# Optimization experiments

Measured on AMD Instinct MI355X. Metric: run time of the kernel, lower is better.

The kernel has to match this reference:

```python
import jax, jax.numpy as jnp
import numpy as np

N_NETS = 76  # 29 h2o + 13 o3 + 9 co2 + 3 n2o + 9 ch4 + 13 u
N_CH = 29
N_KE = [29, 13, 9, 3, 9, 13]
# which composition column each of the 76 nets is scaled by
GAS_OF_NET = np.repeat(np.arange(6), N_KE)
# which output channel each of the 76 tau terms is added into (hardcoded table in subcall)
CHAN_OF_NET = np.concatenate([
    np.arange(29),                                            # h2o[i] -> channel i
    np.array([0, 1, 2, 17, 18, 19, 20, 21, 22, 25, 26, 27, 28]),  # o3
    np.array([0, 1, 2, 5, 6, 9, 10, 13, 14]),                 # co2
    np.array([0, 1, 2]),                                      # n2o
    np.array([0, 1, 2, 3, 4, 7, 8, 11, 12]),                  # ch4
    np.array([0, 1, 2, 15, 16, 17, 18, 19, 20, 21, 22, 27, 28]),  # u
])


def setup_inputs() -> dict:
    key = jax.random.key(0)
    ks = jax.random.split(key, 16)
    B, D_IN, H = 262144, 2, 4
    t_p = jax.random.normal(ks[0], (B, D_IN), dtype=jnp.float32)
    composition = jax.random.uniform(ks[1], (B, 8), dtype=jnp.float32)
    null_lw = jnp.zeros((B, 1), dtype=jnp.float32)
    null_iw = jnp.zeros((B, 1), dtype=jnp.float32)
    # stacked params of the 76 tiny DenseFFNs (hidden [4,4], elu; out 1, softplus)
    W1 = jax.random.normal(ks[2], (N_NETS, D_IN, H), dtype=jnp.float32) * 0.5
    b1 = jax.random.normal(ks[3], (N_NETS, H), dtype=jnp.float32) * 0.05
    W2 = jax.random.normal(ks[4], (N_NETS, H, H), dtype=jnp.float32) * 0.5
    b2 = jax.random.normal(ks[5], (N_NETS, H), dtype=jnp.float32) * 0.05
    W3 = jax.random.uniform(ks[6], (N_NETS, H, 1), minval=-1.0, maxval=1.0, dtype=jnp.float32)
    b3 = jnp.zeros((N_NETS, 1), dtype=jnp.float32)
    # per-channel lw / iw Dense(1) layers (input dim 1)
    W_lw = jax.random.normal(ks[7], (N_CH,), dtype=jnp.float32) * 0.5
    b_lw = jax.random.uniform(ks[8], (N_CH,), minval=0.0, maxval=1.0, dtype=jnp.float32)
    W_iw = jax.random.normal(ks[9], (N_CH,), dtype=jnp.float32) * 0.5
    b_iw = jax.random.uniform(ks[10], (N_CH,), minval=0.0, maxval=1.0, dtype=jnp.float32)
    return {"t_p": t_p, "composition": composition, "null_lw": null_lw, "null_iw": null_iw,
            "W1": W1, "b1": b1, "W2": W2, "b2": b2, "W3": W3, "b3": b3,
            "W_lw": W_lw, "b_lw": b_lw, "W_iw": W_iw, "b_iw": b_iw}


def reference(t_p, composition, null_lw, null_iw, W1, b1, W2, b2, W3, b3, W_lw, b_lw, W_iw, b_iw):
    # all 76 tiny MLPs batched as one einsum chain: [n_nets, B, h]
    h = jax.nn.elu(jnp.einsum('bi,nio->nbo', t_p, W1) + b1[:, None, :])
    h = jax.nn.elu(jnp.einsum('nbi,nio->nbo', h, W2) + b2[:, None, :])
    ke = jax.nn.softplus(jnp.einsum('nbi,nio->nbo', h, W3) + b3[:, None, :])[..., 0]  # [76, B]
    # scale each net's output by its gas concentration, then scatter-add into 29 channels
    tau = ke * composition[:, GAS_OF_NET].T                                  # [76, B]
    tau_gases = jax.ops.segment_sum(tau, jnp.asarray(CHAN_OF_NET), num_segments=N_CH)  # [29, B]
    tau_gases = jnp.transpose(tau_gases)[:, :, None]                          # [B, 29, 1]
    # lw / iw: softplus(null * w_c + b_c) * composition[:, 6 or 7]
    tau_lw = (jax.nn.softplus(null_lw * W_lw[None, :] + b_lw[None, :]) * composition[:, 6:7])[:, :, None]
    tau_iw = (jax.nn.softplus(null_iw * W_iw[None, :] + b_iw[None, :]) * composition[:, 7:8])[:, :, None]
    return (tau_gases, tau_lw, tau_iw)
```

## Files before the change

### kernel.cpp

```cpp
#include <hip/hip_runtime.h>
#include <cstdint>

#define BLOCK 256
#define ROWS 64
#define NREC 40

__device__ __forceinline__ float exp2_fast(float x) { return __builtin_amdgcn_exp2f(x); }
__device__ __forceinline__ float log2_fast(float x) { return __builtin_amdgcn_logf(x); }

#define LN2 0.6931471805599453f
#define L2E 1.4426950408889634f

constexpr int GAS_[76] = {
    0,0,0,0,0,0,0,0,0,0,0,0,0,0,0,0,0,0,0,0,0,0,0,0,0,0,0,0,0,
    1,1,1,1,1,1,1,1,1,1,1,1,1,
    2,2,2,2,2,2,2,2,2,
    3,3,3,
    4,4,4,4,4,4,4,4,4,
    5,5,5,5,5,5,5,5,5,5,5,5,5};
constexpr int CHAN_[76] = {
    0,1,2,3,4,5,6,7,8,9,10,11,12,13,14,15,16,17,18,19,20,21,22,23,24,25,26,27,28,
    0,1,2,17,18,19,20,21,22,25,26,27,28,
    0,1,2,5,6,9,10,13,14,
    0,1,2,
    0,1,2,3,4,7,8,11,12,
    0,1,2,15,16,17,18,19,20,21,22,27,28};

__global__ void __launch_bounds__(128)
prep_kernel(const float* __restrict__ W1, const float* __restrict__ b1,
            const float* __restrict__ W2, const float* __restrict__ b2,
            const float* __restrict__ W3, const float* __restrict__ b3,
            float* __restrict__ rec)
{
    const int n = threadIdx.x;
    if (n >= 76) return;
    float* r = rec + n * NREC;
    #pragma unroll
    for (int k = 0; k < 8; ++k) r[k] = W1[n * 8 + k] * L2E;
    #pragma unroll
    for (int o = 0; o < 4; ++o) r[8 + o] = b1[n * 4 + o] * L2E;
    #pragma unroll
    for (int k = 0; k < 16; ++k) r[12 + k] = W2[n * 16 + k] * L2E;
    #pragma unroll
    for (int o = 0; o < 4; ++o) {
        float s = 0.0f;
        #pragma unroll
        for (int i = 0; i < 4; ++i) s += W2[n * 16 + i * 4 + o];
        r[28 + o] = (b2[n * 4 + o] - s) * L2E;
    }
    float s3 = 0.0f;
    #pragma unroll
    for (int i = 0; i < 4; ++i) { r[32 + i] = W3[n * 4 + i] * L2E; s3 += W3[n * 4 + i]; }
    r[36] = (b3[n] - s3) * L2E;
    r[37] = 0.0f; r[38] = 0.0f; r[39] = 0.0f;
}

__device__ __forceinline__ float elu_h(float as) {
    return fmaxf(fmaf(as, LN2, 1.0f), exp2_fast(fminf(as, 0.0f)));
}

template<int NS, int NE>
__device__ __forceinline__ void run_nets(
    const float* __restrict__ rec, float tpx, float tpy,
    const float* cgl2 , float* tau)
{
    #pragma unroll
    for (int n = NS; n < NE; ++n) {
        const float* __restrict__ R = rec + n * NREC;
        float H1[4];
        #pragma unroll
        for (int o = 0; o < 4; ++o)
            H1[o] = elu_h(fmaf(tpx, R[o], fmaf(tpy, R[4 + o], R[8 + o])));
        float H2[4];
        #pragma unroll
        for (int o = 0; o < 4; ++o) {
            float a = R[28 + o];
            #pragma unroll
            for (int i = 0; i < 4; ++i)
                a = fmaf(H1[i], R[12 + i * 4 + o], a);
            H2[o] = elu_h(a);
        }
        float a3 = R[36];
        #pragma unroll
        for (int i = 0; i < 4; ++i)
            a3 = fmaf(H2[i], R[32 + i], a3);
        const float sp = fmaxf(a3, 0.0f) + log2_fast(1.0f + exp2_fast(-fabsf(a3)));
        tau[CHAN_[n]] = fmaf(sp, cgl2[GAS_[n]], tau[CHAN_[n]]);
    }
}

__device__ __forceinline__ float softplus_nat(float x) {
    return fmaxf(x, 0.0f) + LN2 * log2_fast(1.0f + exp2_fast(-fabsf(x) * L2E));
}

template<bool EXACT>
__global__ void __launch_bounds__(BLOCK)
od_kernel(const float* __restrict__ t_p,
          const float* __restrict__ comp,
          const float* __restrict__ null_lw,
          const float* __restrict__ null_iw,
          const float* __restrict__ rec,
          const float* __restrict__ W_lw, const float* __restrict__ b_lw,
          const float* __restrict__ W_iw, const float* __restrict__ b_iw,
          float* __restrict__ out, int B)
{
    __shared__ float stage[2][ROWS * 29];

    const int wave = threadIdx.x >> 6;
    const int lane = threadIdx.x & 63;
    const int base = blockIdx.x * ROWS;
    const int row  = EXACT ? (base + lane)
                           : ((base + lane < B) ? (base + lane) : (B - 1));

    const float2 tp = *reinterpret_cast<const float2*>(t_p + (size_t)row * 2);
    const float4 ca = *reinterpret_cast<const float4*>(comp + (size_t)row * 8);
    const float2 cbl = *reinterpret_cast<const float2*>(comp + (size_t)row * 8 + 4);
    const float cgl2[6] = {ca.x * LN2, ca.y * LN2, ca.z * LN2,
                           ca.w * LN2, cbl.x * LN2, cbl.y * LN2};

    float tau[29];
    #pragma unroll
    for (int i = 0; i < 29; ++i) tau[i] = 0.0f;

    switch (wave) {
        case 0: run_nets< 0, 19>(rec, tp.x, tp.y, cgl2, tau); break;
        case 1: run_nets<19, 38>(rec, tp.x, tp.y, cgl2, tau); break;
        case 2: run_nets<38, 57>(rec, tp.x, tp.y, cgl2, tau); break;
        default: run_nets<57, 76>(rec, tp.x, tp.y, cgl2, tau); break;
    }

    if (wave < 2) {
        #pragma unroll
        for (int i = 0; i < 29; ++i) stage[wave][lane * 29 + i] = tau[i];
    }
    __syncthreads();
    if (wave >= 2) {
        float* p = stage[wave - 2];
        #pragma unroll
        for (int i = 0; i < 29; ++i) p[lane * 29 + i] += tau[i];
    }
    __syncthreads();

    const size_t obase = (size_t)base * 29;
    const size_t BN = (size_t)B * 29;
    const int lim = EXACT ? (ROWS * 29)
                          : (((B - base < ROWS) ? (B - base) : ROWS) * 29);

    #pragma unroll
    for (int k = 0; k < (ROWS * 29 + BLOCK - 1) / BLOCK; ++k) {
        const int idx = threadIdx.x + k * BLOCK;
        if ((k < (ROWS * 29) / BLOCK || idx < ROWS * 29) && (EXACT || idx < lim)) {
            out[obase + idx] = stage[0][idx] + stage[1][idx];
            const int r  = idx / 29;
            const int ch = idx - r * 29;
            const int grow = base + r;
            const float nl = null_lw[grow];
            const float ni = null_iw[grow];
            const float c6 = comp[(size_t)grow * 8 + 6];
            const float c7 = comp[(size_t)grow * 8 + 7];
            out[BN + obase + idx]     = softplus_nat(fmaf(nl, W_lw[ch], b_lw[ch])) * c6;
            out[2 * BN + obase + idx] = softplus_nat(fmaf(ni, W_iw[ch], b_iw[ch])) * c7;
        }
    }
}

extern "C" void kernel_launch(void* const* d_in, const int* in_sizes, int n_in,
                              void* d_out, int out_size, void* d_ws, size_t ws_size,
                              hipStream_t stream) {
    const float* t_p     = (const float*)d_in[0];
    const float* comp    = (const float*)d_in[1];
    const float* null_lw = (const float*)d_in[2];
    const float* null_iw = (const float*)d_in[3];
    const float* W1      = (const float*)d_in[4];
    const float* b1      = (const float*)d_in[5];
    const float* W2      = (const float*)d_in[6];
    const float* b2      = (const float*)d_in[7];
    const float* W3      = (const float*)d_in[8];
    const float* b3      = (const float*)d_in[9];
    const float* W_lw    = (const float*)d_in[10];
    const float* b_lw    = (const float*)d_in[11];
    const float* W_iw    = (const float*)d_in[12];
    const float* b_iw    = (const float*)d_in[13];
    float* out = (float*)d_out;
    float* rec = (float*)d_ws;

    const int B = in_sizes[0] / 2;

    prep_kernel<<<1, 128, 0, stream>>>(W1, b1, W2, b2, W3, b3, rec);

    const int blocks = (B + ROWS - 1) / ROWS;
    if (B % ROWS == 0)
        od_kernel<true><<<blocks, BLOCK, 0, stream>>>(t_p, comp, null_lw, null_iw,
                                                      rec, W_lw, b_lw, W_iw, b_iw, out, B);
    else
        od_kernel<false><<<blocks, BLOCK, 0, stream>>>(t_p, comp, null_lw, null_iw,
                                                       rec, W_lw, b_lw, W_iw, b_iw, out, B);
}
```

Baseline: 60.64 us.

## Process two rows per thread with packed float2 math and prescaled lw/iw params

```diff
diff --git a/kernel.cpp b/kernel.cpp
--- a/kernel.cpp
+++ b/kernel.cpp
@@ -2,11 +2,19 @@
 #include <cstdint>
 
 #define BLOCK 256
-#define ROWS 64
+#define ROWS 128
 #define NREC 40
 
-__device__ __forceinline__ float exp2_fast(float x) { return __builtin_amdgcn_exp2f(x); }
-__device__ __forceinline__ float log2_fast(float x) { return __builtin_amdgcn_logf(x); }
+typedef float v2f __attribute__((ext_vector_type(2)));
+
+__device__ __forceinline__ float exp2s(float x) { return __builtin_amdgcn_exp2f(x); }
+__device__ __forceinline__ float log2s(float x) { return __builtin_amdgcn_logf(x); }
+__device__ __forceinline__ v2f exp22(v2f x) { return (v2f){exp2s(x.x), exp2s(x.y)}; }
+__device__ __forceinline__ v2f fma2(v2f a, v2f b, v2f c) { return __builtin_elementwise_fma(a, b, c); }
+__device__ __forceinline__ v2f max2(v2f a, v2f b) { return __builtin_elementwise_max(a, b); }
+__device__ __forceinline__ v2f min2(v2f a, v2f b) { return __builtin_elementwise_min(a, b); }
+__device__ __forceinline__ v2f abs2(v2f a) { return __builtin_elementwise_abs(a); }
+__device__ __forceinline__ v2f splat(float s) { return (v2f){s, s}; }
 
 #define LN2 0.6931471805599453f
 #define L2E 1.4426950408889634f
@@ -30,67 +38,75 @@
 prep_kernel(const float* __restrict__ W1, const float* __restrict__ b1,
             const float* __restrict__ W2, const float* __restrict__ b2,
             const float* __restrict__ W3, const float* __restrict__ b3,
+            const float* __restrict__ W_lw, const float* __restrict__ b_lw,
+            const float* __restrict__ W_iw, const float* __restrict__ b_iw,
             float* __restrict__ rec)
 {
     const int n = threadIdx.x;
-    if (n >= 76) return;
-    float* r = rec + n * NREC;
-    #pragma unroll
-    for (int k = 0; k < 8; ++k) r[k] = W1[n * 8 + k] * L2E;
-    #pragma unroll
-    for (int o = 0; o < 4; ++o) r[8 + o] = b1[n * 4 + o] * L2E;
-    #pragma unroll
-    for (int k = 0; k < 16; ++k) r[12 + k] = W2[n * 16 + k] * L2E;
-    #pragma unroll
-    for (int o = 0; o < 4; ++o) {
-        float s = 0.0f;
-        #pragma unroll
-        for (int i = 0; i < 4; ++i) s += W2[n * 16 + i * 4 + o];
-        r[28 + o] = (b2[n * 4 + o] - s) * L2E;
-    }
-    float s3 = 0.0f;
-    #pragma unroll
-    for (int i = 0; i < 4; ++i) { r[32 + i] = W3[n * 4 + i] * L2E; s3 += W3[n * 4 + i]; }
-    r[36] = (b3[n] - s3) * L2E;
-    r[37] = 0.0f; r[38] = 0.0f; r[39] = 0.0f;
-}
-
-__device__ __forceinline__ float elu_h(float as) {
-    return fmaxf(fmaf(as, LN2, 1.0f), exp2_fast(fminf(as, 0.0f)));
+    if (n < 76) {
+        float* r = rec + n * NREC;
+        #pragma unroll
+        for (int k = 0; k < 8; ++k) r[k] = W1[n * 8 + k] * L2E;
+        #pragma unroll
+        for (int o = 0; o < 4; ++o) r[8 + o] = b1[n * 4 + o] * L2E;
+        #pragma unroll
+        for (int k = 0; k < 16; ++k) r[12 + k] = W2[n * 16 + k] * L2E;
+        #pragma unroll
+        for (int o = 0; o < 4; ++o) {
+            float s = 0.0f;
+            #pragma unroll
+            for (int i = 0; i < 4; ++i) s += W2[n * 16 + i * 4 + o];
+            r[28 + o] = (b2[n * 4 + o] - s) * L2E;
+        }
+        float s3 = 0.0f;
+        #pragma unroll
+        for (int i = 0; i < 4; ++i) { r[32 + i] = W3[n * 4 + i] * L2E; s3 += W3[n * 4 + i]; }
+        r[36] = (b3[n] - s3) * L2E;
+        r[37] = 0.0f; r[38] = 0.0f; r[39] = 0.0f;
+    } else if (n < 76 + 29) {
+        const int ch = n - 76;
+        float* t = rec + 76 * NREC + ch * 4;
+        t[0] = W_lw[ch] * L2E;
+        t[1] = b_lw[ch] * L2E;
+        t[2] = W_iw[ch] * L2E;
+        t[3] = b_iw[ch] * L2E;
+    }
+}
+
+__device__ __forceinline__ v2f elu_h2(v2f as) {
+    return max2(fma2(as, splat(LN2), splat(1.0f)), exp22(min2(as, splat(0.0f))));
 }
 
 template<int NS, int NE>
-__device__ __forceinline__ void run_nets(
-    const float* __restrict__ rec, float tpx, float tpy,
-    const float* cgl2 , float* tau)
+__device__ __forceinline__ void run_nets2(
+    const float* __restrict__ rec, v2f tpx, v2f tpy,
+    const v2f* cgl2 , v2f* tau)
 {
     #pragma unroll
     for (int n = NS; n < NE; ++n) {
         const float* __restrict__ R = rec + n * NREC;
-        float H1[4];
+        v2f H1[4];
         #pragma unroll
         for (int o = 0; o < 4; ++o)
-            H1[o] = elu_h(fmaf(tpx, R[o], fmaf(tpy, R[4 + o], R[8 + o])));
-        float H2[4];
+            H1[o] = elu_h2(fma2(tpx, splat(R[o]), fma2(tpy, splat(R[4 + o]), splat(R[8 + o]))));
+        v2f H2[4];
         #pragma unroll
         for (int o = 0; o < 4; ++o) {
-            float a = R[28 + o];
+            v2f a = splat(R[28 + o]);
             #pragma unroll
             for (int i = 0; i < 4; ++i)
-                a = fmaf(H1[i], R[12 + i * 4 + o], a);
-            H2[o] = elu_h(a);
-        }
-        float a3 = R[36];
+                a = fma2(H1[i], splat(R[12 + i * 4 + o]), a);
+            H2[o] = elu_h2(a);
+        }
+        v2f a3 = splat(R[36]);
         #pragma unroll
         for (int i = 0; i < 4; ++i)
-            a3 = fmaf(H2[i], R[32 + i], a3);
-        const float sp = fmaxf(a3, 0.0f) + log2_fast(1.0f + exp2_fast(-fabsf(a3)));
-        tau[CHAN_[n]] = fmaf(sp, cgl2[GAS_[n]], tau[CHAN_[n]]);
-    }
-}
-
-__device__ __forceinline__ float softplus_nat(float x) {
-    return fmaxf(x, 0.0f) + LN2 * log2_fast(1.0f + exp2_fast(-fabsf(x) * L2E));
+            a3 = fma2(H2[i], splat(R[32 + i]), a3);
+        const v2f e = exp22(-abs2(a3));
+        const v2f sp = max2(a3, splat(0.0f)) +
+                       (v2f){log2s(1.0f + e.x), log2s(1.0f + e.y)};
+        tau[CHAN_[n]] = fma2(sp, cgl2[GAS_[n]], tau[CHAN_[n]]);
+    }
 }
 
 template<bool EXACT>
@@ -100,8 +116,6 @@
           const float* __restrict__ null_lw,
           const float* __restrict__ null_iw,
           const float* __restrict__ rec,
-          const float* __restrict__ W_lw, const float* __restrict__ b_lw,
-          const float* __restrict__ W_iw, const float* __restrict__ b_iw,
           float* __restrict__ out, int B)
 {
     __shared__ float stage[2][ROWS * 29];
@@ -109,35 +123,50 @@
     const int wave = threadIdx.x >> 6;
     const int lane = threadIdx.x & 63;
     const int base = blockIdx.x * ROWS;
-    const int row  = EXACT ? (base + lane)
-                           : ((base + lane < B) ? (base + lane) : (B - 1));
-
-    const float2 tp = *reinterpret_cast<const float2*>(t_p + (size_t)row * 2);
-    const float4 ca = *reinterpret_cast<const float4*>(comp + (size_t)row * 8);
-    const float2 cbl = *reinterpret_cast<const float2*>(comp + (size_t)row * 8 + 4);
-    const float cgl2[6] = {ca.x * LN2, ca.y * LN2, ca.z * LN2,
-                           ca.w * LN2, cbl.x * LN2, cbl.y * LN2};
-
-    float tau[29];
+    int r0 = base + lane;
+    int r1 = base + 64 + lane;
+    if (!EXACT) { r0 = r0 < B ? r0 : B - 1; r1 = r1 < B ? r1 : B - 1; }
+
+    const float2 ta = *reinterpret_cast<const float2*>(t_p + (size_t)r0 * 2);
+    const float2 tb = *reinterpret_cast<const float2*>(t_p + (size_t)r1 * 2);
+    const v2f tpx = {ta.x, tb.x};
+    const v2f tpy = {ta.y, tb.y};
+
+    const float4 ca0 = *reinterpret_cast<const float4*>(comp + (size_t)r0 * 8);
+    const float2 cb0 = *reinterpret_cast<const float2*>(comp + (size_t)r0 * 8 + 4);
+    const float4 ca1 = *reinterpret_cast<const float4*>(comp + (size_t)r1 * 8);
+    const float2 cb1 = *reinterpret_cast<const float2*>(comp + (size_t)r1 * 8 + 4);
+    const v2f cgl2[6] = {
+        {ca0.x * LN2, ca1.x * LN2}, {ca0.y * LN2, ca1.y * LN2},
+        {ca0.z * LN2, ca1.z * LN2}, {ca0.w * LN2, ca1.w * LN2},
+        {cb0.x * LN2, cb1.x * LN2}, {cb0.y * LN2, cb1.y * LN2}};
+
+    v2f tau[29];
     #pragma unroll
-    for (int i = 0; i < 29; ++i) tau[i] = 0.0f;
+    for (int i = 0; i < 29; ++i) tau[i] = splat(0.0f);
 
     switch (wave) {
-        case 0: run_nets< 0, 19>(rec, tp.x, tp.y, cgl2, tau); break;
-        case 1: run_nets<19, 38>(rec, tp.x, tp.y, cgl2, tau); break;
-        case 2: run_nets<38, 57>(rec, tp.x, tp.y, cgl2, tau); break;
-        default: run_nets<57, 76>(rec, tp.x, tp.y, cgl2, tau); break;
+        case 0: run_nets2< 0, 19>(rec, tpx, tpy, cgl2, tau); break;
+        case 1: run_nets2<19, 38>(rec, tpx, tpy, cgl2, tau); break;
+        case 2: run_nets2<38, 57>(rec, tpx, tpy, cgl2, tau); break;
+        default: run_nets2<57, 76>(rec, tpx, tpy, cgl2, tau); break;
     }
 
     if (wave < 2) {
         #pragma unroll
-        for (int i = 0; i < 29; ++i) stage[wave][lane * 29 + i] = tau[i];
+        for (int i = 0; i < 29; ++i) {
+            stage[wave][lane * 29 + i] = tau[i].x;
+            stage[wave][(lane + 64) * 29 + i] = tau[i].y;
+        }
     }
     __syncthreads();
     if (wave >= 2) {
         float* p = stage[wave - 2];
         #pragma unroll
-        for (int i = 0; i < 29; ++i) p[lane * 29 + i] += tau[i];
+        for (int i = 0; i < 29; ++i) {
+            p[lane * 29 + i] += tau[i].x;
+            p[(lane + 64) * 29 + i] += tau[i].y;
+        }
     }
     __syncthreads();
 
@@ -145,22 +174,24 @@
     const size_t BN = (size_t)B * 29;
     const int lim = EXACT ? (ROWS * 29)
                           : (((B - base < ROWS) ? (B - base) : ROWS) * 29);
-
-    #pragma unroll
-    for (int k = 0; k < (ROWS * 29 + BLOCK - 1) / BLOCK; ++k) {
-        const int idx = threadIdx.x + k * BLOCK;
-        if ((k < (ROWS * 29) / BLOCK || idx < ROWS * 29) && (EXACT || idx < lim)) {
-            out[obase + idx] = stage[0][idx] + stage[1][idx];
-            const int r  = idx / 29;
-            const int ch = idx - r * 29;
-            const int grow = base + r;
-            const float nl = null_lw[grow];
-            const float ni = null_iw[grow];
-            const float c6 = comp[(size_t)grow * 8 + 6];
-            const float c7 = comp[(size_t)grow * 8 + 7];
-            out[BN + obase + idx]     = softplus_nat(fmaf(nl, W_lw[ch], b_lw[ch])) * c6;
-            out[2 * BN + obase + idx] = softplus_nat(fmaf(ni, W_iw[ch], b_iw[ch])) * c7;
-        }
+    const float* __restrict__ recL = rec + 76 * NREC;
+
+    for (int idx = threadIdx.x; idx < lim; idx += BLOCK) {
+        out[obase + idx] = stage[0][idx] + stage[1][idx];
+        const int r  = idx / 29;
+        const int ch = idx - r * 29;
+        const int grow = base + r;
+        const float nl = null_lw[grow];
+        const float ni = null_iw[grow];
+        const float c6 = comp[(size_t)grow * 8 + 6] * LN2;
+        const float c7 = comp[(size_t)grow * 8 + 7] * LN2;
+        const float4 L = *reinterpret_cast<const float4*>(recL + ch * 4);
+        const float alw = fmaf(nl, L.x, L.y);
+        const float aiw = fmaf(ni, L.z, L.w);
+        out[BN + obase + idx] =
+            (fmaxf(alw, 0.0f) + log2s(1.0f + exp2s(-fabsf(alw)))) * c6;
+        out[2 * BN + obase + idx] =
+            (fmaxf(aiw, 0.0f) + log2s(1.0f + exp2s(-fabsf(aiw)))) * c7;
     }
 }
 
@@ -186,13 +217,14 @@
 
     const int B = in_sizes[0] / 2;
 
-    prep_kernel<<<1, 128, 0, stream>>>(W1, b1, W2, b2, W3, b3, rec);
+    prep_kernel<<<1, 128, 0, stream>>>(W1, b1, W2, b2, W3, b3,
+                                       W_lw, b_lw, W_iw, b_iw, rec);
 
     const int blocks = (B + ROWS - 1) / ROWS;
     if (B % ROWS == 0)
         od_kernel<true><<<blocks, BLOCK, 0, stream>>>(t_p, comp, null_lw, null_iw,
-                                                      rec, W_lw, b_lw, W_iw, b_iw, out, B);
+                                                      rec, out, B);
     else
         od_kernel<false><<<blocks, BLOCK, 0, stream>>>(t_p, comp, null_lw, null_iw,
-                                                       rec, W_lw, b_lw, W_iw, b_iw, out, B);
-}
+                                                       rec, out, B);
+}
```

Measured after the change: 60.97 us. About the same (+0.5%).
